# Optimization experiments

Measured on AMD Instinct MI355X. Metric: run time of the kernel, lower is better.

Reference implementation:

```python
import jax, jax.numpy as jnp
import numpy as np

N_NODES = 100000
N_EDGES = 1600000
N_FEATURES = 128
N_TEMPLATES = 8
N_TEMPLATE_NODES = 8
N_OUTER = 5      # outer FGW (mirror-descent) iterations
N_SINKHORN = 20  # inner Sinkhorn iterations
EPS_REL = 0.05   # entropic reg relative to mean cost magnitude


def setup_inputs() -> dict:
    key = jax.random.key(0)
    k1, k2, k3, k4, k5 = jax.random.split(key, 5)
    x = jax.random.normal(k1, (N_NODES, N_FEATURES), dtype=jnp.float32)
    edge_index = jax.random.randint(k2, (2, N_EDGES), 0, N_NODES, dtype=jnp.int32)
    templates = jax.random.normal(k3, (N_TEMPLATES, N_TEMPLATE_NODES, N_TEMPLATE_NODES), dtype=jnp.float32)
    template_features = jax.random.normal(k4, (N_TEMPLATES, N_TEMPLATE_NODES, N_FEATURES), dtype=jnp.float32)
    q0 = jax.random.normal(k5, (N_TEMPLATES, N_TEMPLATE_NODES), dtype=jnp.float32)
    alpha0 = jnp.zeros((1,), dtype=jnp.float32)
    return {"x": x, "edge_index": edge_index, "templates": templates,
            "template_features": template_features, "q0": q0, "alpha0": alpha0}


def _fgw_forward(x, edge_index, templates, template_features, q0, alpha0):
    # Fused Gromov-Wasserstein distance (square loss) between the input graph
    # (binary adjacency from edge_index, uniform node weights p) and each
    # learned template (C2=templates[k], features, weights q[k]).
    # Inner OT subproblem solved with log-domain Sinkhorn (entropic FGW).
    N, F = x.shape
    K, m, _ = templates.shape
    src, dst = edge_index[0], edge_index[1]
    alpha = jax.nn.sigmoid(alpha0)[0]          # trade-off, scalar
    q = jax.nn.softmax(q0, axis=1)             # [K, m] template node weights
    p = jnp.full((N,), 1.0 / N, dtype=x.dtype) # uniform graph node weights

    def spmm(T):
        # C1 @ T[k] for all templates using the edge list (never densify C1).
        # T: [K, N, m] -> [K, N, m]
        flat = jnp.transpose(T, (1, 0, 2)).reshape(N, K * m)
        out = jax.ops.segment_sum(flat[dst], src, num_segments=N)
        return jnp.transpose(out.reshape(N, K, m), (1, 0, 2))

    # constC for square loss: (C1^2 @ p) 1^T + 1 (C2^2 @ q)^T ; C1 binary so C1^2 = C1
    C1p = jax.ops.segment_sum(p[dst], src, num_segments=N)               # [N]
    constC = C1p[None, :, None] + jnp.einsum('kij,kj->ki', templates ** 2, q)[:, None, :]  # [K,N,m]

    # feature cost: squared euclidean  [K, N, m]
    Mfeat = (jnp.sum(x ** 2, axis=1)[None, :, None]
             + jnp.sum(template_features ** 2, axis=-1)[:, None, :]
             - 2.0 * jnp.einsum('nf,kmf->knm', x, template_features))

    logp = jnp.log(p)
    logq = jnp.log(q)

    def sinkhorn(cost):
        # log-domain Sinkhorn, batched over templates. cost: [K, N, m]
        eps = EPS_REL * jnp.mean(jnp.abs(cost), axis=(1, 2), keepdims=True)  # [K,1,1]
        e = eps[:, :, 0]  # [K,1]

        def body(carry, _):
            f, g = carry
            g = e * logq - e * jax.scipy.special.logsumexp((f[:, :, None] - cost) / eps, axis=1)
            f = e * logp[None, :] - e * jax.scipy.special.logsumexp((g[:, None, :] - cost) / eps, axis=2)
            return (f, g), None

        f0 = jnp.zeros((K, N), cost.dtype)
        g0 = jnp.zeros((K, m), cost.dtype)
        (f, g), _ = jax.lax.scan(body, (f0, g0), None, length=N_SINKHORN)
        return jnp.exp((f[:, :, None] + g[:, None, :] - cost) / eps)

    def gw_tens(T):
        # tens(T) = constC - C1 @ T @ (2*C2)^T  (square-loss GW tensor product)
        CT = spmm(T)
        return constC - 2.0 * jnp.einsum('knm,kpm->knp', CT, templates)

    def outer(T, _):
        cost = alpha * gw_tens(T) + (1.0 - alpha) * Mfeat
        return sinkhorn(cost), None

    T0 = p[None, :, None] * q[:, None, :]  # product-measure init
    T, _ = jax.lax.scan(outer, T0, None, length=N_OUTER)

    tens = gw_tens(T)
    fgw = ((1.0 - alpha) * jnp.sum(Mfeat * T, axis=(1, 2))
           + alpha * jnp.sum(tens * T, axis=(1, 2)))
    return fgw  # [K] FGW distance to each template


def reference(x, edge_index, templates, template_features, q0, alpha0):
    return _fgw_forward(x, edge_index, templates, template_features, q0, alpha0)
```

## Files before the change

kernel.cpp:

```cpp
#include <hip/hip_runtime.h>
#include <math.h>

#define NN 100000
#define NE 1600000
#define NFD 128
#define KT 8
#define MT 8
#define KM 64
#define NOUT 5
#define NSK 20
#define EPSR 0.05f

#define NBLK 248
#define RPBM 404
#define SLOTS 26
#define SCAN_B 391

typedef unsigned int u32;
typedef unsigned long long u64;

__device__ __forceinline__ float groupmax8(float v){
  v = fmaxf(v, __shfl_xor(v,1));
  v = fmaxf(v, __shfl_xor(v,2));
  v = fmaxf(v, __shfl_xor(v,4));
  return v;
}
__device__ __forceinline__ float groupsum8(float v){
  v += __shfl_xor(v,1);
  v += __shfl_xor(v,2);
  v += __shfl_xor(v,4);
  return v;
}
__device__ __forceinline__ float ex2(float x){ return __builtin_amdgcn_exp2f(x); }
__device__ __forceinline__ float lg2(float x){ return __builtin_amdgcn_logf(x); }

__device__ __forceinline__ u64 packMS(float M, float S){
  return ((u64)__builtin_bit_cast(u32, S) << 32) | (u64)__builtin_bit_cast(u32, M);
}
__device__ __forceinline__ float unpackM(u64 v){ return __builtin_bit_cast(float, (u32)(v & 0xffffffffull)); }
__device__ __forceinline__ float unpackS(u64 v){ return __builtin_bit_cast(float, (u32)(v >> 32)); }

__device__ __forceinline__ void gbar(u32* __restrict__ flags, u32 tgt, bool full){
  asm volatile("s_waitcnt vmcnt(0)" ::: "memory");
  __syncthreads();
  const int t = threadIdx.x;
  if (t==0){
    if (full) __builtin_amdgcn_fence(__ATOMIC_RELEASE, "agent");
    __hip_atomic_store(&flags[blockIdx.x], tgt, __ATOMIC_RELAXED, __HIP_MEMORY_SCOPE_AGENT);
  }
  if (t < NBLK){
    int sp = 0;
    while (__hip_atomic_load(&flags[t], __ATOMIC_RELAXED, __HIP_MEMORY_SCOPE_AGENT) < tgt){
      __builtin_amdgcn_s_sleep(2);
      if (++sp > (1<<20)) break;
    }
  }
  __syncthreads();
  if (full){
    if (t==0) __builtin_amdgcn_fence(__ATOMIC_ACQUIRE, "agent");
    __syncthreads();
  }
}

__global__ void k_prep(const float* __restrict__ tmpl, const float* __restrict__ tf,
                       const float* __restrict__ q0, const float* __restrict__ a0,
                       float* __restrict__ qbuf){
  int l = threadIdx.x;
  float z = q0[l];
  float mx = groupmax8(z);
  float ex = expf(z-mx);
  float s  = groupsum8(ex);
  float q  = ex/s;
  float lq = (z-mx) - logf(s);
  float w2q=0.f, tq=0.f;
  int base = l & 56;
  #pragma unroll
  for (int m=0;m<MT;m++){
    float qm = __shfl(q, base+m);
    float tm = tmpl[l*MT+m];
    w2q += tm*tm*qm;
    tq  += tm*qm;
  }
  qbuf[l]=q; qbuf[64+l]=lq; qbuf[128+l]=w2q; qbuf[192+l]=tq;
  if (l==0) qbuf[320] = 1.f/(1.f+expf(-a0[0]));
}

__global__ void k_deg(const int* __restrict__ src, int* __restrict__ deg, int* __restrict__ rank){
  int i = blockIdx.x*blockDim.x + threadIdx.x;
  if (i < NE) rank[i] = atomicAdd(&deg[src[i]], 1);
}
__global__ void k_scan1(const int* __restrict__ deg, int* __restrict__ estart, int* __restrict__ bsum){
  __shared__ int sh[256];
  int t = threadIdx.x, b = blockIdx.x, i = b*256+t;
  int v = (i<NN)? deg[i] : 0;
  sh[t] = v; __syncthreads();
  for (int off=1; off<256; off<<=1){
    int x = (t>=off)? sh[t-off] : 0;
    __syncthreads();
    sh[t] += x;
    __syncthreads();
  }
  if (i<NN) estart[i] = sh[t]-v;
  if (t==255) bsum[b] = sh[t];
}
__global__ void k_scan2(const int* __restrict__ bsum, int* __restrict__ boff){
  __shared__ int sh[512];
  int t = threadIdx.x;
  int v = (t<SCAN_B)? bsum[t] : 0;
  sh[t]=v; __syncthreads();
  for (int off=1; off<512; off<<=1){
    int x = (t>=off)? sh[t-off] : 0;
    __syncthreads();
    sh[t]+=x;
    __syncthreads();
  }
  if (t<SCAN_B) boff[t] = sh[t]-v;
}
__global__ void k_scan3(int* __restrict__ estart, const int* __restrict__ boff){
  int i = blockIdx.x*256 + threadIdx.x;
  if (i<NN) estart[i] += boff[blockIdx.x];
}
__global__ void k_scatter(const int* __restrict__ src, const int* __restrict__ dst,
                          const int* __restrict__ estart, const int* __restrict__ rank,
                          int* __restrict__ sdst){
  int i = blockIdx.x*blockDim.x + threadIdx.x;
  if (i < NE){
    sdst[estart[src[i]] + rank[i]] = dst[i];
  }
}

__global__ void __launch_bounds__(256,2) k_mfeat(const float* __restrict__ x,
                                                 const float* __restrict__ tf,
                                                 float* __restrict__ Mf){
  int t=threadIdx.x, w=t>>6, l=t&63;
  float tfr[NFD];
  #pragma unroll
  for (int j=0;j<NFD;j++) tfr[j]=tf[l*NFD+j];
  float tt=0.f;
  #pragma unroll
  for (int j=0;j<NFD;j++) tt += tfr[j]*tfr[j];
  int gw=blockIdx.x*4+w, nw=gridDim.x*4;
  for (int n=gw; n<NN; n+=nw){
    float x0=x[(size_t)n*NFD+l], x1=x[(size_t)n*NFD+64+l];
    float acc=0.f;
    #pragma unroll
    for (int j=0;j<64;j++){
      float xa=__builtin_bit_cast(float, __builtin_amdgcn_readlane(__builtin_bit_cast(int,x0), j));
      float xb=__builtin_bit_cast(float, __builtin_amdgcn_readlane(__builtin_bit_cast(int,x1), j));
      acc = fmaf(xa, tfr[j], acc);
      acc = fmaf(xb, tfr[64+j], acc);
    }
    float xx=x0*x0+x1*x1;
    xx+=__shfl_xor(xx,1); xx+=__shfl_xor(xx,2); xx+=__shfl_xor(xx,4);
    xx+=__shfl_xor(xx,8); xx+=__shfl_xor(xx,16); xx+=__shfl_xor(xx,32);
    Mf[(size_t)n*KM+l]=xx+tt-2.f*acc;
  }
}

__global__ void __launch_bounds__(1024,4) k_main(
    const float* __restrict__ tmpl, const float* __restrict__ qbuf,
    const int* __restrict__ deg, const int* __restrict__ estart,
    const int* __restrict__ sdst, const float* __restrict__ Mf,
    float* __restrict__ Tg, u64* __restrict__ pb,
    float* __restrict__ absum, float* __restrict__ fgwacc,
    u32* __restrict__ flags, float* __restrict__ outp)
{
  __shared__ float cls[RPBM*KM];
  __shared__ float shm[16*64];
  __shared__ float shs[16*64];
  __shared__ float gsh[64];

  const int t = threadIdx.x, w = t>>6, l = t&63, b = blockIdx.x;
  const int base = l&56;
  const int n0 = b*RPBM;
  const int nrows = min(RPBM, NN-n0);
  const float LOG2E = 1.4426950408889634f;
  const float logp2 = -log2f((float)NN);
  u32 bar = 0;

  float tm[MT];
  #pragma unroll
  for (int m=0;m<MT;m++) tm[m]=tmpl[l*MT+m];
  const float w2q=qbuf[128+l], tq=qbuf[192+l], lq2=qbuf[64+l]*LOG2E, alpha=qbuf[320];
  const float onea = 1.f-alpha;

  float ctreg[SLOTS];
  #pragma unroll
  for (int s=0;s<SLOTS;s++) ctreg[s]=0.f;

  for (int it=0; it<NOUT; ++it){
    float absacc=0.f;
    #pragma unroll
    for (int s=0;s<SLOTS;s++){
      int rr = w + 16*s;
      if (rr < nrows){
        int n = n0+rr;
        float c1p = (float)deg[n]*(1.f/NN);
        float mf = Mf[(size_t)n*KM+l];
        float gwt;
        if (it==0){
          gwt = c1p + w2q - 2.f*c1p*tq;
        } else {
          float ct = ctreg[s];
          float dot=0.f;
          #pragma unroll
          for(int m=0;m<MT;m++) dot += __shfl(ct, base+m)*tm[m];
          gwt = c1p + w2q - 2.f*dot;
        }
        float c = alpha*gwt + onea*mf;
        cls[rr*KM+l]=c;
        absacc += fabsf(c);
      }
    }
    absacc = groupsum8(absacc);
    __syncthreads();
    shm[w*64+l]=absacc;
    __syncthreads();
    if (t<64 && (l&7)==0){
      float v=0.f;
      #pragma unroll
      for(int ww=0;ww<16;ww++) v+=shm[ww*64+l];
      atomicAdd(&absum[it*8+(l>>3)], v);
    }
    gbar(flags, ++bar, false);
    float e = EPSR * __hip_atomic_load(&absum[it*8+(l>>3)], __ATOMIC_RELAXED, __HIP_MEMORY_SCOPE_AGENT)
                   * (1.f/((float)NN*MT));
    float ie2 = LOG2E/e;
    #pragma unroll
    for (int s=0;s<SLOTS;s++){
      int rr = w + 16*s;
      if (rr < nrows) cls[rr*KM+l] *= ie2;
    }

    float gl2 = 0.f;
    for (int j=0;j<NSK;j++){
      float mrun=-3e38f, srun=0.f;
      if (j==0){
        #pragma unroll
        for (int s=0;s<SLOTS;s++){
          int rr = w + 16*s;
          if (rr < nrows){
            float xx = -cls[rr*KM+l];
            float nm = fmaxf(mrun, xx);
            srun = srun*ex2(mrun-nm) + ex2(xx-nm);
            mrun = nm;
          }
        }
      } else {
        #pragma unroll
        for (int s=0;s<SLOTS;s++){
          int rr = w + 16*s;
          if (rr < nrows){
            float c2 = cls[rr*KM+l];
            float y = gl2 - c2;
            float mx = groupmax8(y);
            float s8 = groupsum8(ex2(y-mx));
            float xx = logp2 - (mx+lg2(s8)) - c2;
            float nm = fmaxf(mrun, xx);
            srun = srun*ex2(mrun-nm) + ex2(xx-nm);
            mrun = nm;
          }
        }
      }
      __syncthreads();
      shm[w*64+l]=mrun; shs[w*64+l]=srun;
      __syncthreads();
      if (t<64){
        float M=shm[l], S=shs[l];
        #pragma unroll
        for(int ww=1;ww<16;ww++){
          float m2=shm[ww*64+l], s2=shs[ww*64+l];
          float nm=fmaxf(M,m2);
          S = S*ex2(M-nm) + s2*ex2(m2-nm);
          M = nm;
        }
        __hip_atomic_store(&pb[(size_t)(j&1)*NBLK*KM + (size_t)b*KM + l], packMS(M,S),
                           __ATOMIC_RELAXED, __HIP_MEMORY_SCOPE_AGENT);
      }
      gbar(flags, ++bar, false);
      {
        const u64* pbs = pb + (size_t)(j&1)*NBLK*KM;
        float M=-3e38f, S=0.f;
        for (int bb=w; bb<NBLK; bb+=16){
          u64 v = __hip_atomic_load(&pbs[(size_t)bb*KM + l], __ATOMIC_RELAXED, __HIP_MEMORY_SCOPE_AGENT);
          float m2=unpackM(v), s2=unpackS(v);
          float nm=fmaxf(M,m2);
          S = S*ex2(M-nm) + s2*ex2(m2-nm);
          M = nm;
        }
        shm[w*64+l]=M; shs[w*64+l]=S;
        __syncthreads();
        if (t<64){
          float M2=shm[l], S2=shs[l];
          #pragma unroll
          for(int ww=1;ww<16;ww++){
            float m2=shm[ww*64+l], s2=shs[ww*64+l];
            float nm=fmaxf(M2,m2);
            S2 = S2*ex2(M2-nm) + s2*ex2(m2-nm);
            M2 = nm;
          }
          gsh[l] = lq2 - (M2 + lg2(S2));
        }
        __syncthreads();
        gl2 = gsh[l];
      }
    }

    #pragma unroll
    for (int s=0;s<SLOTS;s++){
      int rr = w + 16*s;
      if (rr < nrows){
        int n = n0+rr;
        float c2 = cls[rr*KM+l];
        float y = gl2 - c2;
        float mx = groupmax8(y);
        float s8 = groupsum8(ex2(y-mx));
        float lse = mx + lg2(s8);
        float tv = ex2(logp2 - lse + y);
        cls[rr*KM+l] = tv;
        Tg[(size_t)n*KM+l] = tv;
      }
    }
    gbar(flags, ++bar, true);

    #pragma unroll
    for (int s=0;s<SLOTS;s++){
      int rr = w + 16*s;
      if (rr < nrows){
        int n = n0+rr;
        int st=estart[n], len=deg[n];
        float acc=0.f;
        int jj=0;
        for (; jj+3<len; jj+=4){
          int d0=sdst[st+jj], d1=sdst[st+jj+1], d2=sdst[st+jj+2], d3=sdst[st+jj+3];
          acc += Tg[(size_t)d0*KM+l]; acc += Tg[(size_t)d1*KM+l];
          acc += Tg[(size_t)d2*KM+l]; acc += Tg[(size_t)d3*KM+l];
        }
        for (; jj<len; jj++) acc += Tg[(size_t)sdst[st+jj]*KM+l];
        ctreg[s]=acc;
      }
    }
  }

  float mfa=0.f, gwa=0.f;
  #pragma unroll
  for (int s=0;s<SLOTS;s++){
    int rr = w + 16*s;
    if (rr < nrows){
      int n = n0+rr;
      float tv = cls[rr*KM+l];
      float mf = Mf[(size_t)n*KM+l];
      float ct = ctreg[s];
      float c1p=(float)deg[n]*(1.f/NN);
      float dot=0.f;
      #pragma unroll
      for(int m=0;m<MT;m++) dot += __shfl(ct, base+m)*tm[m];
      float tens = c1p + w2q - 2.f*dot;
      mfa += mf*tv; gwa += tens*tv;
    }
  }
  mfa=groupsum8(mfa); gwa=groupsum8(gwa);
  __syncthreads();
  shm[w*64+l]=mfa; shs[w*64+l]=gwa;
  __syncthreads();
  if (t<64 && (l&7)==0){
    float vm=0.f, vg=0.f;
    #pragma unroll
    for(int ww=0;ww<16;ww++){ vm+=shm[ww*64+l]; vg+=shs[ww*64+l]; }
    atomicAdd(&fgwacc[l>>3], vm);
    atomicAdd(&fgwacc[8+(l>>3)], vg);
  }
  gbar(flags, ++bar, false);
  if (b==0 && t<8){
    float fm = __hip_atomic_load(&fgwacc[t],   __ATOMIC_RELAXED, __HIP_MEMORY_SCOPE_AGENT);
    float fg = __hip_atomic_load(&fgwacc[8+t], __ATOMIC_RELAXED, __HIP_MEMORY_SCOPE_AGENT);
    outp[t] = onea*fm + alpha*fg;
  }
}

extern "C" void kernel_launch(void* const* d_in, const int* in_sizes, int n_in,
                              void* d_out, int out_size, void* d_ws, size_t ws_size,
                              hipStream_t stream){
  const float* x    = (const float*)d_in[0];
  const int*   ei   = (const int*)  d_in[1];
  const float* tmpl = (const float*)d_in[2];
  const float* tf   = (const float*)d_in[3];
  const float* q0   = (const float*)d_in[4];
  const float* a0   = (const float*)d_in[5];
  const int* src = ei;
  const int* dst = ei + NE;

  char* ws = (char*)d_ws;
  size_t o=0;
  auto carve = [&](size_t bytes)->void*{ void* p = ws+o; o += (bytes+255)&~(size_t)255; return p; };
  float* Tg    = (float*)carve((size_t)NN*KM*4);
  float* Mf    = (float*)carve((size_t)NN*KM*4);
  int* sdst    = (int*)carve((size_t)NE*4);
  int* rank    = (int*)carve((size_t)NE*4);
  int* deg     = (int*)carve((size_t)NN*4);
  int* estart  = (int*)carve((size_t)NN*4);
  int* bsum    = (int*)carve(512*4);
  int* boff    = (int*)carve(512*4);
  float* qbuf  = (float*)carve(512*4);
  float* absum = (float*)carve(64*4);
  float* fgwacc= (float*)carve(64*4);
  u32* flags   = (u32*)carve(NBLK*4);
  u64* pb      = (u64*)carve((size_t)2*NBLK*KM*8);

  hipMemsetAsync(deg,    0, NN*4,    stream);
  hipMemsetAsync(absum,  0, 64*4,    stream);
  hipMemsetAsync(fgwacc, 0, 64*4,    stream);
  hipMemsetAsync(flags,  0, NBLK*4,  stream);

  k_prep<<<1,64,0,stream>>>(tmpl, tf, q0, a0, qbuf);
  k_deg<<<(NE+255)/256,256,0,stream>>>(src, deg, rank);
  k_scan1<<<SCAN_B,256,0,stream>>>(deg, estart, bsum);
  k_scan2<<<1,512,0,stream>>>(bsum, boff);
  k_scan3<<<SCAN_B,256,0,stream>>>(estart, boff);
  k_scatter<<<(NE+255)/256,256,0,stream>>>(src, dst, estart, rank, sdst);
  k_mfeat<<<512,256,0,stream>>>(x, tf, Mf);

  k_main<<<NBLK,1024,0,stream>>>(tmpl, qbuf, deg, estart, sdst, Mf,
                                 Tg, pb, absum, fgwacc, flags, (float*)d_out);
}
```

Measured before the change: 3.132 ms.

## Remap Sinkhorn threads to hold whole row-template tiles in registers

Each thread now handles one (row, template) pair with all 8 template-node costs kept in registers, instead of one lane per cost entry. This removes the cross-lane shuffle reductions for the row log-sum-exp in every Sinkhorn iteration. Block and grid reductions are rebuilt around an XOR-swizzled shared buffer and a branch-light log-sum-exp combine. The global float atomicAdds for the cost-scale and final sums are replaced by per-block partial slots that every block reduces itself. The cost is higher register pressure from the 32 cost values per thread, plus an extra shared-memory staging pass for the Tg writes and the SpMM result.

```diff
diff --git a/kernel.cpp b/kernel.cpp
--- a/kernel.cpp
+++ b/kernel.cpp
@@ -13,7 +13,9 @@
 
 #define NBLK 248
 #define RPBM 404
-#define SLOTS 26
+#define WSLOTS 26
+#define KSLOTS 4
+#define MSST 130
 #define SCAN_B 391
 
 typedef unsigned int u32;
@@ -39,6 +41,13 @@
 }
 __device__ __forceinline__ float unpackM(u64 v){ return __builtin_bit_cast(float, (u32)(v & 0xffffffffull)); }
 __device__ __forceinline__ float unpackS(u64 v){ return __builtin_bit_cast(float, (u32)(v >> 32)); }
+
+__device__ __forceinline__ void lsecomb(float& M, float& S, float m2, float s2){
+  float d = m2 - M;
+  float p = ex2(-fabsf(d));
+  S = (d <= 0.f) ? fmaf(s2, p, S) : fmaf(S, p, s2);
+  M = fmaxf(M, m2);
+}
 
 __device__ __forceinline__ void gbar(u32* __restrict__ flags, u32 tgt, bool full){
   asm volatile("s_waitcnt vmcnt(0)" ::: "memory");
@@ -157,224 +166,312 @@
   }
 }
 
+__device__ __forceinline__ int cidx(int rr, int l){
+  return rr*64 + ((((l>>3) ^ (rr&7))<<3) | (l&7));
+}
+
 __global__ void __launch_bounds__(1024,4) k_main(
     const float* __restrict__ tmpl, const float* __restrict__ qbuf,
     const int* __restrict__ deg, const int* __restrict__ estart,
     const int* __restrict__ sdst, const float* __restrict__ Mf,
     float* __restrict__ Tg, u64* __restrict__ pb,
-    float* __restrict__ absum, float* __restrict__ fgwacc,
+    float* __restrict__ pbabs, float* __restrict__ pbfgw,
     u32* __restrict__ flags, float* __restrict__ outp)
 {
-  __shared__ float cls[RPBM*KM];
-  __shared__ float shm[16*64];
-  __shared__ float shs[16*64];
-  __shared__ float gsh[64];
-
-  const int t = threadIdx.x, w = t>>6, l = t&63, b = blockIdx.x;
-  const int base = l&56;
+  __shared__ __align__(16) float LB[RPBM*KM];
+  __shared__ __align__(16) float gsh[64];
+  __shared__ float lq2sh[64];
+  __shared__ float tlsh[512];
+  __shared__ float esh[8];
+  __shared__ float wred[16];
+  __shared__ float wred2[16];
+
+  const int t = threadIdx.x, b = blockIdx.x;
+  const int w = t>>6, l = t&63;
+  const int k = t>>7, j2 = t&127;
   const int n0 = b*RPBM;
   const int nrows = min(RPBM, NN-n0);
   const float LOG2E = 1.4426950408889634f;
   const float logp2 = -log2f((float)NN);
   u32 bar = 0;
 
-  float tm[MT];
-  #pragma unroll
-  for (int m=0;m<MT;m++) tm[m]=tmpl[l*MT+m];
-  const float w2q=qbuf[128+l], tq=qbuf[192+l], lq2=qbuf[64+l]*LOG2E, alpha=qbuf[320];
-  const float onea = 1.f-alpha;
-
-  float ctreg[SLOTS];
-  #pragma unroll
-  for (int s=0;s<SLOTS;s++) ctreg[s]=0.f;
+  if (t<64) lq2sh[t] = qbuf[64+t]*LOG2E;
+  if (t<512) tlsh[t] = tmpl[t];
+  float w2q8[8], tq8[8];
+  #pragma unroll
+  for (int m=0;m<8;m++){ w2q8[m]=qbuf[128+k*8+m]; tq8[m]=qbuf[192+k*8+m]; }
+  const float alpha=qbuf[320], onea=1.f-alpha;
+  __syncthreads();
+
+  float c2[KSLOTS][8];
+  float g8[8];
+  #pragma unroll
+  for (int m=0;m<8;m++) g8[m]=0.f;
 
   for (int it=0; it<NOUT; ++it){
-    float absacc=0.f;
+    float absacc = 0.f;
     #pragma unroll
-    for (int s=0;s<SLOTS;s++){
-      int rr = w + 16*s;
+    for (int s=0;s<KSLOTS;s++){
+      int rr = j2 + 128*s;
       if (rr < nrows){
         int n = n0+rr;
         float c1p = (float)deg[n]*(1.f/NN);
-        float mf = Mf[(size_t)n*KM+l];
-        float gwt;
-        if (it==0){
-          gwt = c1p + w2q - 2.f*c1p*tq;
-        } else {
-          float ct = ctreg[s];
-          float dot=0.f;
-          #pragma unroll
-          for(int m=0;m<MT;m++) dot += __shfl(ct, base+m)*tm[m];
-          gwt = c1p + w2q - 2.f*dot;
-        }
-        float c = alpha*gwt + onea*mf;
-        cls[rr*KM+l]=c;
-        absacc += fabsf(c);
-      }
-    }
-    absacc = groupsum8(absacc);
-    __syncthreads();
-    shm[w*64+l]=absacc;
-    __syncthreads();
-    if (t<64 && (l&7)==0){
-      float v=0.f;
+        float mv[8];
+        { const float4* mp = (const float4*)&Mf[(size_t)n*KM + k*8];
+          *(float4*)&mv[0] = mp[0]; *(float4*)&mv[4] = mp[1]; }
+        float ct[8];
+        if (it>0){
+          const float4* cp = (const float4*)&LB[rr*64 + ((k ^ (rr&7))<<3)];
+          *(float4*)&ct[0] = cp[0]; *(float4*)&ct[4] = cp[1];
+        }
+        #pragma unroll
+        for (int p=0;p<8;p++){
+          float gwt;
+          if (it==0){
+            gwt = c1p + w2q8[p] - 2.f*c1p*tq8[p];
+          } else {
+            float dot=0.f;
+            #pragma unroll
+            for (int m=0;m<8;m++) dot = fmaf(ct[m], tlsh[k*64+p*8+m], dot);
+            gwt = c1p + w2q8[p] - 2.f*dot;
+          }
+          float c = alpha*gwt + onea*mv[p];
+          c2[s][p] = c;
+          absacc += fabsf(c);
+        }
+      }
+    }
+    #pragma unroll
+    for (int d=1; d<64; d<<=1) absacc += __shfl_xor(absacc, d);
+    __syncthreads();
+    if ((t&63)==0) wred[w] = absacc;
+    __syncthreads();
+    if (t<8)
+      __hip_atomic_store(&pbabs[(size_t)(it*NBLK+b)*8 + t], wred[2*t]+wred[2*t+1],
+                         __ATOMIC_RELAXED, __HIP_MEMORY_SCOPE_AGENT);
+    gbar(flags, ++bar, false);
+    {
+      int k0 = t&7, i = t>>3;
+      float v = 0.f;
+      if (i < NBLK)
+        v += __hip_atomic_load(&pbabs[(size_t)(it*NBLK+i)*8+k0], __ATOMIC_RELAXED, __HIP_MEMORY_SCOPE_AGENT);
+      if (i+128 < NBLK)
+        v += __hip_atomic_load(&pbabs[(size_t)(it*NBLK+i+128)*8+k0], __ATOMIC_RELAXED, __HIP_MEMORY_SCOPE_AGENT);
+      LB[i*9+k0] = v;
+      __syncthreads();
       #pragma unroll
-      for(int ww=0;ww<16;ww++) v+=shm[ww*64+l];
-      atomicAdd(&absum[it*8+(l>>3)], v);
-    }
-    gbar(flags, ++bar, false);
-    float e = EPSR * __hip_atomic_load(&absum[it*8+(l>>3)], __ATOMIC_RELAXED, __HIP_MEMORY_SCOPE_AGENT)
-                   * (1.f/((float)NN*MT));
-    float ie2 = LOG2E/e;
-    #pragma unroll
-    for (int s=0;s<SLOTS;s++){
-      int rr = w + 16*s;
-      if (rr < nrows) cls[rr*KM+l] *= ie2;
-    }
-
-    float gl2 = 0.f;
-    for (int j=0;j<NSK;j++){
-      float mrun=-3e38f, srun=0.f;
-      if (j==0){
-        #pragma unroll
-        for (int s=0;s<SLOTS;s++){
-          int rr = w + 16*s;
-          if (rr < nrows){
-            float xx = -cls[rr*KM+l];
-            float nm = fmaxf(mrun, xx);
-            srun = srun*ex2(mrun-nm) + ex2(xx-nm);
-            mrun = nm;
+      for (int off=64; off>=1; off>>=1){
+        if (i < off) LB[i*9+k0] += LB[(i+off)*9+k0];
+        __syncthreads();
+      }
+      if (t<8) esh[t] = EPSR * LB[t] * (1.f/((float)NN*MT));
+      __syncthreads();
+    }
+    {
+      float ie2 = LOG2E / esh[k];
+      #pragma unroll
+      for (int s=0;s<KSLOTS;s++)
+        #pragma unroll
+        for (int p=0;p<8;p++) c2[s][p] *= ie2;
+    }
+
+    for (int jj=0; jj<NSK; ++jj){
+      float M8[8], S8[8];
+      #pragma unroll
+      for (int m=0;m<8;m++){ M8[m]=-3e38f; S8[m]=0.f; }
+      if (jj==0){
+        #pragma unroll
+        for (int s=0;s<KSLOTS;s++){
+          int rr = j2+128*s;
+          if (rr<nrows){
+            #pragma unroll
+            for (int m=0;m<8;m++) lsecomb(M8[m], S8[m], -c2[s][m], 1.f);
           }
         }
       } else {
         #pragma unroll
-        for (int s=0;s<SLOTS;s++){
-          int rr = w + 16*s;
-          if (rr < nrows){
-            float c2 = cls[rr*KM+l];
-            float y = gl2 - c2;
-            float mx = groupmax8(y);
-            float s8 = groupsum8(ex2(y-mx));
-            float xx = logp2 - (mx+lg2(s8)) - c2;
-            float nm = fmaxf(mrun, xx);
-            srun = srun*ex2(mrun-nm) + ex2(xx-nm);
-            mrun = nm;
+        for (int s=0;s<KSLOTS;s++){
+          int rr = j2+128*s;
+          if (rr<nrows){
+            float y[8];
+            #pragma unroll
+            for (int m=0;m<8;m++) y[m] = g8[m] - c2[s][m];
+            float mx = fmaxf(fmaxf(fmaxf(y[0],y[1]),fmaxf(y[2],y[3])),
+                             fmaxf(fmaxf(y[4],y[5]),fmaxf(y[6],y[7])));
+            float sr = 0.f;
+            #pragma unroll
+            for (int m=0;m<8;m++) sr += ex2(y[m]-mx);
+            float base = logp2 - (mx + lg2(sr));
+            #pragma unroll
+            for (int m=0;m<8;m++) lsecomb(M8[m], S8[m], base - c2[s][m], 1.f);
           }
         }
       }
+      float* msM = LB;
+      float* msS = LB + 64*MSST;
+      #pragma unroll
+      for (int m=0;m<8;m++){
+        msM[(k*8+m)*MSST + j2] = M8[m];
+        msS[(k*8+m)*MSST + j2] = S8[m];
+      }
       __syncthreads();
-      shm[w*64+l]=mrun; shs[w*64+l]=srun;
-      __syncthreads();
-      if (t<64){
-        float M=shm[l], S=shs[l];
-        #pragma unroll
-        for(int ww=1;ww<16;ww++){
-          float m2=shm[ww*64+l], s2=shs[ww*64+l];
-          float nm=fmaxf(M,m2);
-          S = S*ex2(M-nm) + s2*ex2(m2-nm);
-          M = nm;
-        }
-        __hip_atomic_store(&pb[(size_t)(j&1)*NBLK*KM + (size_t)b*KM + l], packMS(M,S),
-                           __ATOMIC_RELAXED, __HIP_MEMORY_SCOPE_AGENT);
+      {
+        int c = t>>4, sub = t&15;
+        float M=-3e38f, S=0.f;
+        #pragma unroll
+        for (int i=0;i<8;i++){
+          int ji = sub + 16*i;
+          lsecomb(M, S, msM[c*MSST+ji], msS[c*MSST+ji]);
+        }
+        #pragma unroll
+        for (int d=1; d<16; d<<=1){
+          float m2 = __shfl_xor(M, d);
+          float s2 = __shfl_xor(S, d);
+          lsecomb(M, S, m2, s2);
+        }
+        if (sub==0)
+          __hip_atomic_store(&pb[(size_t)(jj&1)*NBLK*KM + (size_t)b*KM + c], packMS(M,S),
+                             __ATOMIC_RELAXED, __HIP_MEMORY_SCOPE_AGENT);
       }
       gbar(flags, ++bar, false);
       {
-        const u64* pbs = pb + (size_t)(j&1)*NBLK*KM;
+        const u64* pbs = pb + (size_t)(jj&1)*NBLK*KM;
+        int c = t&63, ch = t>>6;
         float M=-3e38f, S=0.f;
-        for (int bb=w; bb<NBLK; bb+=16){
-          u64 v = __hip_atomic_load(&pbs[(size_t)bb*KM + l], __ATOMIC_RELAXED, __HIP_MEMORY_SCOPE_AGENT);
-          float m2=unpackM(v), s2=unpackS(v);
-          float nm=fmaxf(M,m2);
-          S = S*ex2(M-nm) + s2*ex2(m2-nm);
-          M = nm;
-        }
-        shm[w*64+l]=M; shs[w*64+l]=S;
+        #pragma unroll
+        for (int half=0; half<2; half++){
+          u64 vv[8];
+          #pragma unroll
+          for (int i=0;i<8;i++){
+            int bb = ch*16 + half*8 + i;
+            vv[i] = (bb<NBLK) ? __hip_atomic_load(&pbs[(size_t)bb*KM + c], __ATOMIC_RELAXED, __HIP_MEMORY_SCOPE_AGENT)
+                              : packMS(-3e38f, 0.f);
+          }
+          #pragma unroll
+          for (int i=0;i<8;i++) lsecomb(M, S, unpackM(vv[i]), unpackS(vv[i]));
+        }
+        u64* xch = (u64*)LB;
+        xch[c*16 + ch] = packMS(M,S);
         __syncthreads();
         if (t<64){
-          float M2=shm[l], S2=shs[l];
+          float M2=-3e38f, S2=0.f;
           #pragma unroll
-          for(int ww=1;ww<16;ww++){
-            float m2=shm[ww*64+l], s2=shs[ww*64+l];
-            float nm=fmaxf(M2,m2);
-            S2 = S2*ex2(M2-nm) + s2*ex2(m2-nm);
-            M2 = nm;
+          for (int i=0;i<16;i++){
+            u64 v2 = xch[t*16+i];
+            lsecomb(M2, S2, unpackM(v2), unpackS(v2));
           }
-          gsh[l] = lq2 - (M2 + lg2(S2));
+          gsh[t] = lq2sh[t] - (M2 + lg2(S2));
         }
         __syncthreads();
-        gl2 = gsh[l];
-      }
+      }
+      #pragma unroll
+      for (int m=0;m<8;m++) g8[m] = gsh[k*8+m];
     }
 
     #pragma unroll
-    for (int s=0;s<SLOTS;s++){
-      int rr = w + 16*s;
-      if (rr < nrows){
-        int n = n0+rr;
-        float c2 = cls[rr*KM+l];
-        float y = gl2 - c2;
-        float mx = groupmax8(y);
-        float s8 = groupsum8(ex2(y-mx));
-        float lse = mx + lg2(s8);
-        float tv = ex2(logp2 - lse + y);
-        cls[rr*KM+l] = tv;
-        Tg[(size_t)n*KM+l] = tv;
-      }
+    for (int s=0;s<KSLOTS;s++){
+      int rr = j2+128*s;
+      if (rr<nrows){
+        float y[8];
+        #pragma unroll
+        for (int m=0;m<8;m++) y[m] = g8[m] - c2[s][m];
+        float mx = fmaxf(fmaxf(fmaxf(y[0],y[1]),fmaxf(y[2],y[3])),
+                         fmaxf(fmaxf(y[4],y[5]),fmaxf(y[6],y[7])));
+        float sr = 0.f;
+        #pragma unroll
+        for (int m=0;m<8;m++) sr += ex2(y[m]-mx);
+        float base = logp2 - (mx + lg2(sr));
+        #pragma unroll
+        for (int m=0;m<8;m++) c2[s][m] = ex2(base + y[m]);
+        float4* dp = (float4*)&LB[rr*64 + ((k ^ (rr&7))<<3)];
+        dp[0] = make_float4(c2[s][0],c2[s][1],c2[s][2],c2[s][3]);
+        dp[1] = make_float4(c2[s][4],c2[s][5],c2[s][6],c2[s][7]);
+      }
+    }
+    __syncthreads();
+    for (int s2=0;s2<WSLOTS;s2++){
+      int rr2 = w + 16*s2;
+      if (rr2<nrows) Tg[(size_t)(n0+rr2)*KM + l] = LB[cidx(rr2,l)];
     }
     gbar(flags, ++bar, true);
 
-    #pragma unroll
-    for (int s=0;s<SLOTS;s++){
-      int rr = w + 16*s;
-      if (rr < nrows){
-        int n = n0+rr;
+    for (int s2=0;s2<WSLOTS;s2++){
+      int rr2 = w + 16*s2;
+      if (rr2<nrows){
+        int n = n0+rr2;
         int st=estart[n], len=deg[n];
         float acc=0.f;
-        int jj=0;
-        for (; jj+3<len; jj+=4){
-          int d0=sdst[st+jj], d1=sdst[st+jj+1], d2=sdst[st+jj+2], d3=sdst[st+jj+3];
+        int e=0;
+        for (; e+3<len; e+=4){
+          int d0=sdst[st+e], d1=sdst[st+e+1], d2=sdst[st+e+2], d3=sdst[st+e+3];
           acc += Tg[(size_t)d0*KM+l]; acc += Tg[(size_t)d1*KM+l];
           acc += Tg[(size_t)d2*KM+l]; acc += Tg[(size_t)d3*KM+l];
         }
-        for (; jj<len; jj++) acc += Tg[(size_t)sdst[st+jj]*KM+l];
-        ctreg[s]=acc;
-      }
-    }
-  }
-
-  float mfa=0.f, gwa=0.f;
-  #pragma unroll
-  for (int s=0;s<SLOTS;s++){
-    int rr = w + 16*s;
-    if (rr < nrows){
+        for (; e<len; e++) acc += Tg[(size_t)sdst[st+e]*KM+l];
+        LB[cidx(rr2,l)] = acc;
+      }
+    }
+    __syncthreads();
+  }
+
+  float mfacc=0.f, gwacc=0.f;
+  #pragma unroll
+  for (int s=0;s<KSLOTS;s++){
+    int rr = j2+128*s;
+    if (rr<nrows){
       int n = n0+rr;
-      float tv = cls[rr*KM+l];
-      float mf = Mf[(size_t)n*KM+l];
-      float ct = ctreg[s];
-      float c1p=(float)deg[n]*(1.f/NN);
-      float dot=0.f;
+      float c1p = (float)deg[n]*(1.f/NN);
+      float mv[8];
+      { const float4* mp = (const float4*)&Mf[(size_t)n*KM + k*8];
+        *(float4*)&mv[0]=mp[0]; *(float4*)&mv[4]=mp[1]; }
+      float ct[8];
+      { const float4* cp = (const float4*)&LB[rr*64 + ((k ^ (rr&7))<<3)];
+        *(float4*)&ct[0]=cp[0]; *(float4*)&ct[4]=cp[1]; }
       #pragma unroll
-      for(int m=0;m<MT;m++) dot += __shfl(ct, base+m)*tm[m];
-      float tens = c1p + w2q - 2.f*dot;
-      mfa += mf*tv; gwa += tens*tv;
-    }
-  }
-  mfa=groupsum8(mfa); gwa=groupsum8(gwa);
+      for (int p=0;p<8;p++){
+        float dot=0.f;
+        #pragma unroll
+        for (int m=0;m<8;m++) dot = fmaf(ct[m], tlsh[k*64+p*8+m], dot);
+        float tens = c1p + w2q8[p] - 2.f*dot;
+        mfacc = fmaf(mv[p], c2[s][p], mfacc);
+        gwacc = fmaf(tens, c2[s][p], gwacc);
+      }
+    }
+  }
+  #pragma unroll
+  for (int d=1; d<64; d<<=1){ mfacc += __shfl_xor(mfacc,d); gwacc += __shfl_xor(gwacc,d); }
   __syncthreads();
-  shm[w*64+l]=mfa; shs[w*64+l]=gwa;
+  if ((t&63)==0){ wred[w]=mfacc; wred2[w]=gwacc; }
   __syncthreads();
-  if (t<64 && (l&7)==0){
+  if (t<8){
+    __hip_atomic_store(&pbfgw[((size_t)b*8+t)*2+0], wred[2*t]+wred[2*t+1],
+                       __ATOMIC_RELAXED, __HIP_MEMORY_SCOPE_AGENT);
+    __hip_atomic_store(&pbfgw[((size_t)b*8+t)*2+1], wred2[2*t]+wred2[2*t+1],
+                       __ATOMIC_RELAXED, __HIP_MEMORY_SCOPE_AGENT);
+  }
+  gbar(flags, ++bar, false);
+  if (b==0){
+    int k0 = t&7, i = t>>3;
     float vm=0.f, vg=0.f;
+    if (i < NBLK){
+      vm += __hip_atomic_load(&pbfgw[((size_t)i*8+k0)*2+0], __ATOMIC_RELAXED, __HIP_MEMORY_SCOPE_AGENT);
+      vg += __hip_atomic_load(&pbfgw[((size_t)i*8+k0)*2+1], __ATOMIC_RELAXED, __HIP_MEMORY_SCOPE_AGENT);
+    }
+    if (i+128 < NBLK){
+      vm += __hip_atomic_load(&pbfgw[((size_t)(i+128)*8+k0)*2+0], __ATOMIC_RELAXED, __HIP_MEMORY_SCOPE_AGENT);
+      vg += __hip_atomic_load(&pbfgw[((size_t)(i+128)*8+k0)*2+1], __ATOMIC_RELAXED, __HIP_MEMORY_SCOPE_AGENT);
+    }
+    LB[i*9+k0] = vm; LB[1280 + i*9+k0] = vg;
+    __syncthreads();
     #pragma unroll
-    for(int ww=0;ww<16;ww++){ vm+=shm[ww*64+l]; vg+=shs[ww*64+l]; }
-    atomicAdd(&fgwacc[l>>3], vm);
-    atomicAdd(&fgwacc[8+(l>>3)], vg);
-  }
-  gbar(flags, ++bar, false);
-  if (b==0 && t<8){
-    float fm = __hip_atomic_load(&fgwacc[t],   __ATOMIC_RELAXED, __HIP_MEMORY_SCOPE_AGENT);
-    float fg = __hip_atomic_load(&fgwacc[8+t], __ATOMIC_RELAXED, __HIP_MEMORY_SCOPE_AGENT);
-    outp[t] = onea*fm + alpha*fg;
+    for (int off=64; off>=1; off>>=1){
+      if (i < off){
+        LB[i*9+k0]      += LB[(i+off)*9+k0];
+        LB[1280+i*9+k0] += LB[1280+(i+off)*9+k0];
+      }
+      __syncthreads();
+    }
+    if (t<8) outp[t] = onea*LB[t] + alpha*LB[1280+t];
   }
 }
 
@@ -402,15 +499,13 @@
   int* bsum    = (int*)carve(512*4);
   int* boff    = (int*)carve(512*4);
   float* qbuf  = (float*)carve(512*4);
-  float* absum = (float*)carve(64*4);
-  float* fgwacc= (float*)carve(64*4);
   u32* flags   = (u32*)carve(NBLK*4);
   u64* pb      = (u64*)carve((size_t)2*NBLK*KM*8);
-
-  hipMemsetAsync(deg,    0, NN*4,    stream);
-  hipMemsetAsync(absum,  0, 64*4,    stream);
-  hipMemsetAsync(fgwacc, 0, 64*4,    stream);
-  hipMemsetAsync(flags,  0, NBLK*4,  stream);
+  float* pbabs = (float*)carve((size_t)NOUT*NBLK*8*4);
+  float* pbfgw = (float*)carve((size_t)NBLK*16*4);
+
+  hipMemsetAsync(deg,   0, NN*4,   stream);
+  hipMemsetAsync(flags, 0, NBLK*4, stream);
 
   k_prep<<<1,64,0,stream>>>(tmpl, tf, q0, a0, qbuf);
   k_deg<<<(NE+255)/256,256,0,stream>>>(src, deg, rank);
@@ -421,5 +516,5 @@
   k_mfeat<<<512,256,0,stream>>>(x, tf, Mf);
 
   k_main<<<NBLK,1024,0,stream>>>(tmpl, qbuf, deg, estart, sdst, Mf,
-                                 Tg, pb, absum, fgwacc, flags, (float*)d_out);
-}
+                                 Tg, pb, pbabs, pbfgw, flags, (float*)d_out);
+}
```

New measurement: 2.999 ms. -4.2%, faster.
